# Performance work log

Measured on AMD Instinct MI355X. Metric: run time of the kernel, lower is better.

## Reference

```python
import jax, jax.numpy as jnp
import numpy as np

B = 32768   # batch
D = 64      # latent_dimension_half
H = 256     # inner_dimension
T = D * (D + 1) // 2  # 2080 triangular outputs


def setup_inputs() -> dict:
    key = jax.random.key(0)
    ks = jax.random.split(key, 7)
    s = 0.05
    return {
        "x": jax.random.normal(ks[0], (B, D), dtype=jnp.float32),
        "W1": jax.random.normal(ks[1], (D, H), dtype=jnp.float32) * s,
        "b1": jax.random.normal(ks[2], (H,), dtype=jnp.float32) * s,
        "W2": jax.random.normal(ks[3], (H, H), dtype=jnp.float32) * s,
        "b2": jax.random.normal(ks[4], (H,), dtype=jnp.float32) * s,
        "W3": jax.random.normal(ks[5], (H, T), dtype=jnp.float32) * s,
        "b3": jax.random.normal(ks[6], (T,), dtype=jnp.float32) * s,
    }


def reference(x, W1, b1, W2, b2, W3, b3):
    d = x.shape[-1]  # latent_dimension_half
    h = jnp.tanh(x @ W1 + b1)
    h = jnp.tanh(h @ W2 + b2)
    t = jnp.tanh(h @ W3 + b3)  # [B, d*(d+1)/2]
    # scatter: first d entries -> diagonal (diagflat), rest -> strict upper
    # triangle in row-major order (matches torch boolean-mask assignment)
    di = np.arange(d)
    iu, ju = np.triu_indices(d, k=1)
    rows = np.concatenate([di, iu])
    cols = np.concatenate([di, ju])
    u = jnp.zeros((x.shape[0], d, d), dtype=t.dtype).at[:, rows, cols].set(t)
    # y[b] = u[b].T @ u[b]
    return jnp.einsum('bki,bkj->bij', u, u)
```

## Files before the change

### kernel.cpp

```cpp
#include <hip/hip_runtime.h>


typedef __bf16 bf16_t;
typedef bf16_t bf16x8 __attribute__((ext_vector_type(8)));
typedef float  f32x4  __attribute__((ext_vector_type(4)));

#define MFMA16(a, b, c) __builtin_amdgcn_mfma_f32_16x16x32_bf16((a), (b), (c), 0, 0, 0)

constexpr int SLOT  = 4608;
constexpr int H2OFF = 147456;

__device__ __forceinline__ float fast_tanh(float x) {
  float cx = fminf(fmaxf(x, -30.0f), 30.0f);
  float t  = __expf(2.0f * cx);
  return (t - 1.0f) * __builtin_amdgcn_rcpf(t + 1.0f);
}

__device__ __forceinline__ bf16x8 zsel(bf16x8 f, bool keep) {
  union { bf16x8 v; unsigned int u[4]; } x;
  x.v = f;
  unsigned m = keep ? 0xFFFFFFFFu : 0u;
#pragma unroll
  for (int p = 0; p < 4; ++p) x.u[p] &= m;
  return x.v;
}

__device__ __forceinline__ void decode_p(int p, int& j, int& k) {
  int cc = p >> 3, e = p & 7;
  int b = 0;
  while (b < 7 && cc >= 4 * (b + 1) * (b + 2)) ++b;
  int rl  = b + 1;
  int rem = cc - 4 * b * (b + 1);
  j = 8 * b + rem / rl;
  k = (rem % rl) * 8 + e;
}

__global__ void prep_kernel(const float* __restrict__ W1, const float* __restrict__ W2,
                            const float* __restrict__ W3, const float* __restrict__ b3,
                            char* __restrict__ wsb) {
  int tid = blockIdx.x * 512 + threadIdx.x;
  bf16_t* ws = (bf16_t*)wsb;
  if (tid < 16384) {
    int n = tid >> 6, k = tid & 63;
    ws[tid] = (bf16_t)W1[k * 256 + n];
  } else if (tid < 81920) {
    int m = tid - 16384;
    int n = m >> 8, k = m & 255;
    ws[tid] = (bf16_t)W2[k * 256 + n];
  } else if (tid < 671744) {
    int m = tid - 81920;
    int t  = m >> 12;
    int r  = m & 4095;
    int kk = r >> 9;
    int g  = (r >> 7) & 3;
    int c  = (r >> 3) & 15;
    int e  = r & 7;
    int p  = t * 16 + c;
    int k  = kk * 32 + g * 8 + e;
    int j, kd;
    decode_p(p, j, kd);
    float v = 0.f;
    if (kd <= j) {
      int n_ref = (kd == j) ? j : (64 + kd * 63 - (kd * (kd - 1)) / 2 + j - kd - 1);
      v = W3[k * 2080 + n_ref];
    }
    ws[tid] = (bf16_t)v;
  } else if (tid < 674048) {
    int p = tid - 671744;
    int j, kd;
    decode_p(p, j, kd);
    float v = 0.f;
    if (kd <= j) {
      int n_ref = (kd == j) ? j : (64 + kd * 63 - (kd * (kd - 1)) / 2 + j - kd - 1);
      v = b3[n_ref];
    }
    ((float*)(wsb + 1343488))[p] = v;
  }
}

__global__ void __launch_bounds__(1024, 4)
hm_kernel(const float* __restrict__ x, const float* __restrict__ b1,
          const float* __restrict__ b2, const char* __restrict__ wsb,
          float* __restrict__ out) {
  extern __shared__ char smem[];
  const int tid  = threadIdx.x;
  const int w    = tid >> 6;
  const int wv   = w & 7;
  const int mt   = w >> 3;
  const int lane = tid & 63;
  const int g    = lane >> 4;
  const int c    = lane & 15;
  const int blk  = blockIdx.x;

  const bf16_t* W1t = (const bf16_t*)wsb;
  const bf16_t* W2t = W1t + 16384;
  const bf16_t* W3q = W1t + 81920;
  const float*  b3p = (const float*)(wsb + 1343488);

  char* xs  = smem;
  char* h1s = smem + 8192;
  char* h2s = smem + H2OFF;

  if (tid < 512) {
    f32x4 v = *(const f32x4*)(x + (size_t)blk * 2048 + tid * 4);
    int row = tid >> 4, col = (tid & 15) * 4;
    union { bf16_t b[4]; unsigned long long u; } pk;
    pk.b[0] = (bf16_t)v[0]; pk.b[1] = (bf16_t)v[1];
    pk.b[2] = (bf16_t)v[2]; pk.b[3] = (bf16_t)v[3];
    *(unsigned long long*)(xs + ((row * 128 + col * 2) ^ ((row & 7) << 4))) = pk.u;
  }
  __syncthreads();

  {
    int arow = mt * 16 + c;
    bf16x8 a0 = *(const bf16x8*)(xs + ((arow * 128 + g * 16) ^ ((arow & 7) << 4)));
    bf16x8 a1 = *(const bf16x8*)(xs + ((arow * 128 + 64 + g * 16) ^ ((arow & 7) << 4)));
#pragma unroll
    for (int ni = 0; ni < 2; ++ni) {
      int n = (wv * 2 + ni) * 16 + c;
      bf16x8 bw0 = *(const bf16x8*)(W1t + n * 64 + g * 8);
      bf16x8 bw1 = *(const bf16x8*)(W1t + n * 64 + 32 + g * 8);
      f32x4 acc = {0.f, 0.f, 0.f, 0.f};
      acc = MFMA16(a0, bw0, acc);
      acc = MFMA16(a1, bw1, acc);
      float bias = b1[n];
#pragma unroll
      for (int r = 0; r < 4; ++r) {
        int row = mt * 16 + g * 4 + r;
        float v = fast_tanh(acc[r] + bias);
        *(bf16_t*)(h1s + ((row * 512 + n * 2) ^ ((row & 7) << 4))) = (bf16_t)v;
      }
    }
  }
  __syncthreads();

#pragma unroll
  for (int ni = 0; ni < 2; ++ni) {
    int n = (wv * 2 + ni) * 16 + c;
    int arow = mt * 16 + c;
    f32x4 acc0 = {0.f, 0.f, 0.f, 0.f}, acc1 = {0.f, 0.f, 0.f, 0.f};
#pragma unroll
    for (int kk = 0; kk < 8; kk += 2) {
      bf16x8 a0 = *(const bf16x8*)(h1s + ((arow * 512 + kk * 64 + g * 16) ^ ((arow & 7) << 4)));
      bf16x8 a1 = *(const bf16x8*)(h1s + ((arow * 512 + (kk + 1) * 64 + g * 16) ^ ((arow & 7) << 4)));
      bf16x8 bw0 = *(const bf16x8*)(W2t + n * 256 + kk * 32 + g * 8);
      bf16x8 bw1 = *(const bf16x8*)(W2t + n * 256 + (kk + 1) * 32 + g * 8);
      acc0 = MFMA16(a0, bw0, acc0);
      acc1 = MFMA16(a1, bw1, acc1);
    }
    f32x4 acc = acc0 + acc1;
    float bias = b2[n];
#pragma unroll
    for (int r = 0; r < 4; ++r) {
      int row = mt * 16 + g * 4 + r;
      float v = fast_tanh(acc[r] + bias);
      *(bf16_t*)(h2s + ((row * 512 + n * 2) ^ ((row & 7) << 4))) = (bf16_t)v;
    }
  }
  __syncthreads();

  {
    int arow = mt * 16 + c;
    bf16x8 a0 = *(const bf16x8*)(h2s + ((arow * 512 + 0 * 64 + g * 16) ^ ((arow & 7) << 4)));
    bf16x8 a1 = *(const bf16x8*)(h2s + ((arow * 512 + 1 * 64 + g * 16) ^ ((arow & 7) << 4)));
    bf16x8 a2 = *(const bf16x8*)(h2s + ((arow * 512 + 2 * 64 + g * 16) ^ ((arow & 7) << 4)));
    bf16x8 a3 = *(const bf16x8*)(h2s + ((arow * 512 + 3 * 64 + g * 16) ^ ((arow & 7) << 4)));
    bf16x8 a4 = *(const bf16x8*)(h2s + ((arow * 512 + 4 * 64 + g * 16) ^ ((arow & 7) << 4)));
    bf16x8 a5 = *(const bf16x8*)(h2s + ((arow * 512 + 5 * 64 + g * 16) ^ ((arow & 7) << 4)));
    bf16x8 a6 = *(const bf16x8*)(h2s + ((arow * 512 + 6 * 64 + g * 16) ^ ((arow & 7) << 4)));
    bf16x8 a7 = *(const bf16x8*)(h2s + ((arow * 512 + 7 * 64 + g * 16) ^ ((arow & 7) << 4)));

    char* tw = smem + (mt * 16 + g * 4) * SLOT;
    const int swz = ((mt * 4 + g) & 7) << 4;

    bf16x8 A0, A1, A2, A3, A4, A5, A6, A7; float Ab;
    bf16x8 B0, B1, B2, B3, B4, B5, B6, B7; float Bb;

#define ISSUE_T(S, TI)                                                              \
  do {                                                                              \
    int t_ = wv + (TI) * 8;                                                         \
    const bf16_t* np_ = W3q + t_ * 4096 + lane * 8;                                 \
    asm volatile("global_load_dwordx4 %0, %1, off" : "=v"(S##0) : "v"(np_));            \
    asm volatile("global_load_dwordx4 %0, %1, off" : "=v"(S##1) : "v"(np_ + 512));      \
    asm volatile("global_load_dwordx4 %0, %1, off" : "=v"(S##2) : "v"(np_ + 1024));     \
    asm volatile("global_load_dwordx4 %0, %1, off" : "=v"(S##3) : "v"(np_ + 1536));     \
    asm volatile("global_load_dwordx4 %0, %1, off" : "=v"(S##4) : "v"(np_ + 2048));     \
    asm volatile("global_load_dwordx4 %0, %1, off" : "=v"(S##5) : "v"(np_ + 2560));     \
    asm volatile("global_load_dwordx4 %0, %1, off" : "=v"(S##6) : "v"(np_ + 3072));     \
    asm volatile("global_load_dwordx4 %0, %1, off" : "=v"(S##7) : "v"(np_ + 3584));     \
    asm volatile("global_load_dword %0, %1, off"   : "=v"(S##b) : "v"(b3p + t_ * 16 + c)); \
  } while (0)

#define WAIT_N(N)                                          \
  do {                                                     \
    asm volatile("s_waitcnt vmcnt(" #N ")" ::: "memory");  \
    __builtin_amdgcn_sched_barrier(0);                     \
  } while (0)

#define COMP_T(S, TI)                                                    \
  do {                                                                   \
    f32x4 acc0 = {S##b, S##b, S##b, S##b};                               \
    f32x4 acc1 = {0.f, 0.f, 0.f, 0.f};                                   \
    acc0 = MFMA16(a0, S##0, acc0); acc1 = MFMA16(a1, S##1, acc1);        \
    acc0 = MFMA16(a2, S##2, acc0); acc1 = MFMA16(a3, S##3, acc1);        \
    acc0 = MFMA16(a4, S##4, acc0); acc1 = MFMA16(a5, S##5, acc1);        \
    acc0 = MFMA16(a6, S##6, acc0); acc1 = MFMA16(a7, S##7, acc1);        \
    f32x4 accs = acc0 + acc1;                                            \
    int p_ = (wv + (TI) * 8) * 16 + c;                                   \
    _Pragma("unroll")                                                    \
    for (int r_ = 0; r_ < 4; ++r_) {                                     \
      float v_ = fast_tanh(accs[r_]);                                    \
      *(bf16_t*)(tw + r_ * SLOT + ((p_ * 2) ^ swz)) = (bf16_t)v_;        \
    }                                                                    \
  } while (0)

    ISSUE_T(A, 0);
#pragma unroll 1
    for (int pr = 0; pr < 8; ++pr) {
      ISSUE_T(B, 2 * pr + 1);
      WAIT_N(9);
      COMP_T(A, 2 * pr);
      ISSUE_T(A, 2 * pr + 2);
      WAIT_N(9);
      COMP_T(B, 2 * pr + 1);
    }
    ISSUE_T(B, 17);
    WAIT_N(9);
    COMP_T(A, 16);
    WAIT_N(0);
    COMP_T(B, 17);

#undef ISSUE_T
#undef WAIT_N
#undef COMP_T
  }
  __syncthreads();

#pragma unroll
  for (int bi = 0; bi < 2; ++bi) {
    int m = w * 2 + bi;
    char* slot = smem + m * SLOT;
    const int sw = ((m >> 2) & 7) << 4;

    bf16x8 f0, f1, f2, f3, f2b, f3b;
#pragma unroll
    for (int ti = 0; ti < 4; ++ti) {
      int j = ti * 16 + c;
      int Q = j >> 3, s = j & 7;
      int ro = 16 * (4 * Q * (Q + 1) + s * (Q + 1));
      bf16x8 fa = *(const bf16x8*)(slot + ((ro + g * 16) ^ sw));
      if (ti == 0) f0 = zsel(fa, g * 8 <= j);
      if (ti == 1) f1 = zsel(fa, g * 8 <= j);
      if (ti == 2) f2 = fa;
      if (ti == 3) f3 = fa;
      if (ti >= 2) {
        bf16x8 fb = *(const bf16x8*)(slot + ((ro + 64 + g * 16) ^ sw));
        fb = zsel(fb, 32 + g * 8 <= j);
        if (ti == 2) f2b = fb;
        else         f3b = fb;
      }
    }

    bf16x8 fA[4] = {f0, f1, f2, f3};
    f32x4 acc[4][4];
#pragma unroll
    for (int ti = 0; ti < 4; ++ti)
#pragma unroll
      for (int tj = 0; tj < 4; ++tj) {
        f32x4 z = {0.f, 0.f, 0.f, 0.f};
        acc[ti][tj] = MFMA16(fA[ti], fA[tj], z);
      }
    acc[2][2] = MFMA16(f2b, f2b, acc[2][2]);
    acc[2][3] = MFMA16(f2b, f3b, acc[2][3]);
    acc[3][2] = MFMA16(f3b, f2b, acc[3][2]);
    acc[3][3] = MFMA16(f3b, f3b, acc[3][3]);

    float* yb = out + (size_t)(blk * 32 + m) * 4096;
#pragma unroll
    for (int ti = 0; ti < 4; ++ti) {
#pragma unroll
      for (int tj = 0; tj < 4; ++tj)
#pragma unroll
        for (int r = 0; r < 4; ++r)
          *(float*)(slot + (g * 4 + r) * 256 + (tj * 16 + c) * 4) = acc[ti][tj][r];
#pragma unroll
      for (int ii = 0; ii < 4; ++ii) {
        f32x4 v = *(const f32x4*)(slot + ii * 1024 + lane * 16);
        *(f32x4*)(yb + ti * 1024 + ii * 256 + lane * 4) = v;
      }
    }
  }
}

extern "C" void kernel_launch(void* const* d_in, const int* in_sizes, int n_in,
                              void* d_out, int out_size, void* d_ws, size_t ws_size,
                              hipStream_t stream) {
  (void)in_sizes; (void)n_in; (void)out_size; (void)ws_size;
  const float* x  = (const float*)d_in[0];
  const float* W1 = (const float*)d_in[1];
  const float* b1 = (const float*)d_in[2];
  const float* W2 = (const float*)d_in[3];
  const float* b2 = (const float*)d_in[4];
  const float* W3 = (const float*)d_in[5];
  const float* b3 = (const float*)d_in[6];
  char* wsb = (char*)d_ws;
  float* out = (float*)d_out;

  prep_kernel<<<1317, 512, 0, stream>>>(W1, W2, W3, b3, wsb);

  hipFuncSetAttribute((const void*)hm_kernel,
                      hipFuncAttributeMaxDynamicSharedMemorySize, 163840);
  hm_kernel<<<1024, 1024, 163840, stream>>>(x, b1, b2, wsb, out);
}
```

Measured before the change: 213.9 us.

## Halve block to 512 threads, each wave computing both 16-row M tiles

Blocks shrink from 16 waves to 8, and each wave now covers both 16-row halves of the 32-row batch tile. The W3 B-fragments loaded from global memory are shared between the two MFMA row tiles, so each block fetches half as many W3 bytes per output. The cost is more registers per wave (16 A fragments plus two accumulator sets) and fewer waves to hide latency. Launch bounds change to 512 threads with minimum 2 blocks.

```diff
diff --git a/kernel.cpp b/kernel.cpp
--- a/kernel.cpp
+++ b/kernel.cpp
@@ -78,15 +78,13 @@
   }
 }
 
-__global__ void __launch_bounds__(1024, 4)
+__global__ void __launch_bounds__(512, 2)
 hm_kernel(const float* __restrict__ x, const float* __restrict__ b1,
           const float* __restrict__ b2, const char* __restrict__ wsb,
           float* __restrict__ out) {
   extern __shared__ char smem[];
   const int tid  = threadIdx.x;
   const int w    = tid >> 6;
-  const int wv   = w & 7;
-  const int mt   = w >> 3;
   const int lane = tid & 63;
   const int g    = lane >> 4;
   const int c    = lane & 15;
@@ -101,7 +99,7 @@
   char* h1s = smem + 8192;
   char* h2s = smem + H2OFF;
 
-  if (tid < 512) {
+  {
     f32x4 v = *(const f32x4*)(x + (size_t)blk * 2048 + tid * 4);
     int row = tid >> 4, col = (tid & 15) * 4;
     union { bf16_t b[4]; unsigned long long u; } pk;
@@ -111,13 +109,14 @@
   }
   __syncthreads();
 
-  {
+#pragma unroll
+  for (int mt = 0; mt < 2; ++mt) {
     int arow = mt * 16 + c;
     bf16x8 a0 = *(const bf16x8*)(xs + ((arow * 128 + g * 16) ^ ((arow & 7) << 4)));
     bf16x8 a1 = *(const bf16x8*)(xs + ((arow * 128 + 64 + g * 16) ^ ((arow & 7) << 4)));
 #pragma unroll
     for (int ni = 0; ni < 2; ++ni) {
-      int n = (wv * 2 + ni) * 16 + c;
+      int n = (w * 2 + ni) * 16 + c;
       bf16x8 bw0 = *(const bf16x8*)(W1t + n * 64 + g * 8);
       bf16x8 bw1 = *(const bf16x8*)(W1t + n * 64 + 32 + g * 8);
       f32x4 acc = {0.f, 0.f, 0.f, 0.f};
@@ -135,50 +134,63 @@
   __syncthreads();
 
 #pragma unroll
-  for (int ni = 0; ni < 2; ++ni) {
-    int n = (wv * 2 + ni) * 16 + c;
+  for (int mt = 0; mt < 2; ++mt) {
     int arow = mt * 16 + c;
-    f32x4 acc0 = {0.f, 0.f, 0.f, 0.f}, acc1 = {0.f, 0.f, 0.f, 0.f};
-#pragma unroll
-    for (int kk = 0; kk < 8; kk += 2) {
-      bf16x8 a0 = *(const bf16x8*)(h1s + ((arow * 512 + kk * 64 + g * 16) ^ ((arow & 7) << 4)));
-      bf16x8 a1 = *(const bf16x8*)(h1s + ((arow * 512 + (kk + 1) * 64 + g * 16) ^ ((arow & 7) << 4)));
-      bf16x8 bw0 = *(const bf16x8*)(W2t + n * 256 + kk * 32 + g * 8);
-      bf16x8 bw1 = *(const bf16x8*)(W2t + n * 256 + (kk + 1) * 32 + g * 8);
-      acc0 = MFMA16(a0, bw0, acc0);
-      acc1 = MFMA16(a1, bw1, acc1);
-    }
-    f32x4 acc = acc0 + acc1;
-    float bias = b2[n];
-#pragma unroll
-    for (int r = 0; r < 4; ++r) {
-      int row = mt * 16 + g * 4 + r;
-      float v = fast_tanh(acc[r] + bias);
-      *(bf16_t*)(h2s + ((row * 512 + n * 2) ^ ((row & 7) << 4))) = (bf16_t)v;
+#pragma unroll
+    for (int ni = 0; ni < 2; ++ni) {
+      int n = (w * 2 + ni) * 16 + c;
+      f32x4 acc0 = {0.f, 0.f, 0.f, 0.f}, acc1 = {0.f, 0.f, 0.f, 0.f};
+#pragma unroll
+      for (int kk = 0; kk < 8; kk += 2) {
+        bf16x8 a0 = *(const bf16x8*)(h1s + ((arow * 512 + kk * 64 + g * 16) ^ ((arow & 7) << 4)));
+        bf16x8 a1 = *(const bf16x8*)(h1s + ((arow * 512 + (kk + 1) * 64 + g * 16) ^ ((arow & 7) << 4)));
+        bf16x8 bw0 = *(const bf16x8*)(W2t + n * 256 + kk * 32 + g * 8);
+        bf16x8 bw1 = *(const bf16x8*)(W2t + n * 256 + (kk + 1) * 32 + g * 8);
+        acc0 = MFMA16(a0, bw0, acc0);
+        acc1 = MFMA16(a1, bw1, acc1);
+      }
+      f32x4 acc = acc0 + acc1;
+      float bias = b2[n];
+#pragma unroll
+      for (int r = 0; r < 4; ++r) {
+        int row = mt * 16 + g * 4 + r;
+        float v = fast_tanh(acc[r] + bias);
+        *(bf16_t*)(h2s + ((row * 512 + n * 2) ^ ((row & 7) << 4))) = (bf16_t)v;
+      }
     }
   }
   __syncthreads();
 
   {
-    int arow = mt * 16 + c;
-    bf16x8 a0 = *(const bf16x8*)(h2s + ((arow * 512 + 0 * 64 + g * 16) ^ ((arow & 7) << 4)));
-    bf16x8 a1 = *(const bf16x8*)(h2s + ((arow * 512 + 1 * 64 + g * 16) ^ ((arow & 7) << 4)));
-    bf16x8 a2 = *(const bf16x8*)(h2s + ((arow * 512 + 2 * 64 + g * 16) ^ ((arow & 7) << 4)));
-    bf16x8 a3 = *(const bf16x8*)(h2s + ((arow * 512 + 3 * 64 + g * 16) ^ ((arow & 7) << 4)));
-    bf16x8 a4 = *(const bf16x8*)(h2s + ((arow * 512 + 4 * 64 + g * 16) ^ ((arow & 7) << 4)));
-    bf16x8 a5 = *(const bf16x8*)(h2s + ((arow * 512 + 5 * 64 + g * 16) ^ ((arow & 7) << 4)));
-    bf16x8 a6 = *(const bf16x8*)(h2s + ((arow * 512 + 6 * 64 + g * 16) ^ ((arow & 7) << 4)));
-    bf16x8 a7 = *(const bf16x8*)(h2s + ((arow * 512 + 7 * 64 + g * 16) ^ ((arow & 7) << 4)));
-
-    char* tw = smem + (mt * 16 + g * 4) * SLOT;
-    const int swz = ((mt * 4 + g) & 7) << 4;
+    int arowL = c, arowH = 16 + c;
+    bf16x8 aL0 = *(const bf16x8*)(h2s + ((arowL * 512 + 0 * 64 + g * 16) ^ ((arowL & 7) << 4)));
+    bf16x8 aL1 = *(const bf16x8*)(h2s + ((arowL * 512 + 1 * 64 + g * 16) ^ ((arowL & 7) << 4)));
+    bf16x8 aL2 = *(const bf16x8*)(h2s + ((arowL * 512 + 2 * 64 + g * 16) ^ ((arowL & 7) << 4)));
+    bf16x8 aL3 = *(const bf16x8*)(h2s + ((arowL * 512 + 3 * 64 + g * 16) ^ ((arowL & 7) << 4)));
+    bf16x8 aL4 = *(const bf16x8*)(h2s + ((arowL * 512 + 4 * 64 + g * 16) ^ ((arowL & 7) << 4)));
+    bf16x8 aL5 = *(const bf16x8*)(h2s + ((arowL * 512 + 5 * 64 + g * 16) ^ ((arowL & 7) << 4)));
+    bf16x8 aL6 = *(const bf16x8*)(h2s + ((arowL * 512 + 6 * 64 + g * 16) ^ ((arowL & 7) << 4)));
+    bf16x8 aL7 = *(const bf16x8*)(h2s + ((arowL * 512 + 7 * 64 + g * 16) ^ ((arowL & 7) << 4)));
+    bf16x8 aH0 = *(const bf16x8*)(h2s + ((arowH * 512 + 0 * 64 + g * 16) ^ ((arowH & 7) << 4)));
+    bf16x8 aH1 = *(const bf16x8*)(h2s + ((arowH * 512 + 1 * 64 + g * 16) ^ ((arowH & 7) << 4)));
+    bf16x8 aH2 = *(const bf16x8*)(h2s + ((arowH * 512 + 2 * 64 + g * 16) ^ ((arowH & 7) << 4)));
+    bf16x8 aH3 = *(const bf16x8*)(h2s + ((arowH * 512 + 3 * 64 + g * 16) ^ ((arowH & 7) << 4)));
+    bf16x8 aH4 = *(const bf16x8*)(h2s + ((arowH * 512 + 4 * 64 + g * 16) ^ ((arowH & 7) << 4)));
+    bf16x8 aH5 = *(const bf16x8*)(h2s + ((arowH * 512 + 5 * 64 + g * 16) ^ ((arowH & 7) << 4)));
+    bf16x8 aH6 = *(const bf16x8*)(h2s + ((arowH * 512 + 6 * 64 + g * 16) ^ ((arowH & 7) << 4)));
+    bf16x8 aH7 = *(const bf16x8*)(h2s + ((arowH * 512 + 7 * 64 + g * 16) ^ ((arowH & 7) << 4)));
+
+    char* twL = smem + (g * 4) * SLOT;
+    char* twH = smem + (16 + g * 4) * SLOT;
+    const int swzL = (g & 7) << 4;
+    const int swzH = ((4 + g) & 7) << 4;
 
     bf16x8 A0, A1, A2, A3, A4, A5, A6, A7; float Ab;
     bf16x8 B0, B1, B2, B3, B4, B5, B6, B7; float Bb;
 
 #define ISSUE_T(S, TI)                                                              \
   do {                                                                              \
-    int t_ = wv + (TI) * 8;                                                         \
+    int t_ = w + (TI) * 8;                                                          \
     const bf16_t* np_ = W3q + t_ * 4096 + lane * 8;                                 \
     asm volatile("global_load_dwordx4 %0, %1, off" : "=v"(S##0) : "v"(np_));            \
     asm volatile("global_load_dwordx4 %0, %1, off" : "=v"(S##1) : "v"(np_ + 512));      \
@@ -197,21 +209,28 @@
     __builtin_amdgcn_sched_barrier(0);                     \
   } while (0)
 
-#define COMP_T(S, TI)                                                    \
-  do {                                                                   \
-    f32x4 acc0 = {S##b, S##b, S##b, S##b};                               \
-    f32x4 acc1 = {0.f, 0.f, 0.f, 0.f};                                   \
-    acc0 = MFMA16(a0, S##0, acc0); acc1 = MFMA16(a1, S##1, acc1);        \
-    acc0 = MFMA16(a2, S##2, acc0); acc1 = MFMA16(a3, S##3, acc1);        \
-    acc0 = MFMA16(a4, S##4, acc0); acc1 = MFMA16(a5, S##5, acc1);        \
-    acc0 = MFMA16(a6, S##6, acc0); acc1 = MFMA16(a7, S##7, acc1);        \
-    f32x4 accs = acc0 + acc1;                                            \
-    int p_ = (wv + (TI) * 8) * 16 + c;                                   \
-    _Pragma("unroll")                                                    \
-    for (int r_ = 0; r_ < 4; ++r_) {                                     \
-      float v_ = fast_tanh(accs[r_]);                                    \
-      *(bf16_t*)(tw + r_ * SLOT + ((p_ * 2) ^ swz)) = (bf16_t)v_;        \
-    }                                                                    \
+#define COMP_T(S, TI)                                                      \
+  do {                                                                     \
+    f32x4 al0 = {S##b, S##b, S##b, S##b}, al1 = {0.f, 0.f, 0.f, 0.f};      \
+    f32x4 ah0 = {S##b, S##b, S##b, S##b}, ah1 = {0.f, 0.f, 0.f, 0.f};      \
+    al0 = MFMA16(aL0, S##0, al0); al1 = MFMA16(aL1, S##1, al1);            \
+    ah0 = MFMA16(aH0, S##0, ah0); ah1 = MFMA16(aH1, S##1, ah1);            \
+    al0 = MFMA16(aL2, S##2, al0); al1 = MFMA16(aL3, S##3, al1);            \
+    ah0 = MFMA16(aH2, S##2, ah0); ah1 = MFMA16(aH3, S##3, ah1);            \
+    al0 = MFMA16(aL4, S##4, al0); al1 = MFMA16(aL5, S##5, al1);            \
+    ah0 = MFMA16(aH4, S##4, ah0); ah1 = MFMA16(aH5, S##5, ah1);            \
+    al0 = MFMA16(aL6, S##6, al0); al1 = MFMA16(aL7, S##7, al1);            \
+    ah0 = MFMA16(aH6, S##6, ah0); ah1 = MFMA16(aH7, S##7, ah1);            \
+    f32x4 asL = al0 + al1;                                                 \
+    f32x4 asH = ah0 + ah1;                                                 \
+    int p_ = (w + (TI) * 8) * 16 + c;                                      \
+    _Pragma("unroll")                                                      \
+    for (int r_ = 0; r_ < 4; ++r_) {                                       \
+      float vL = fast_tanh(asL[r_]);                                       \
+      *(bf16_t*)(twL + r_ * SLOT + ((p_ * 2) ^ swzL)) = (bf16_t)vL;        \
+      float vH = fast_tanh(asH[r_]);                                       \
+      *(bf16_t*)(twH + r_ * SLOT + ((p_ * 2) ^ swzH)) = (bf16_t)vH;        \
+    }                                                                      \
   } while (0)
 
     ISSUE_T(A, 0);
@@ -237,8 +256,8 @@
   __syncthreads();
 
 #pragma unroll
-  for (int bi = 0; bi < 2; ++bi) {
-    int m = w * 2 + bi;
+  for (int bi = 0; bi < 4; ++bi) {
+    int m = w * 4 + bi;
     char* slot = smem + m * SLOT;
     const int sw = ((m >> 2) & 7) << 4;
 
@@ -310,5 +329,5 @@
 
   hipFuncSetAttribute((const void*)hm_kernel,
                       hipFuncAttributeMaxDynamicSharedMemorySize, 163840);
-  hm_kernel<<<1024, 1024, 163840, stream>>>(x, b1, b2, wsb, out);
-}
+  hm_kernel<<<1024, 512, 163840, stream>>>(x, b1, b2, wsb, out);
+}
```

Result: faster. 184.8 us (-13.6%).
